# Performance work log

Hardware: AMD Instinct MI355X
Metric: run time of the kernel (lower is better)

Reference implementation:

```python
import jax, jax.numpy as jnp
import numpy as np

B, T, C = 16, 2048, 512
G = 2                 # groups
V = 320               # num_vars
D = C // G            # var_dim = 256
GAMMA = 0.25
GN_EPS = 1e-5


def setup_inputs() -> dict:
    key = jax.random.key(0)
    k1, k2, k3 = jax.random.split(key, 3)
    x = jax.random.normal(k1, (B, T, C), dtype=jnp.float32)
    # grouped 1x1 conv weight: (out_channels, in_channels_per_group) = (C, D)
    conv_w = jax.random.normal(k2, (C, D), dtype=jnp.float32) * (1.0 / np.sqrt(D))
    gn_w = jnp.ones((C,), dtype=jnp.float32)
    gn_b = jnp.zeros((C,), dtype=jnp.float32)
    embedding = 0.01 * jax.random.normal(k3, (V, G, D), dtype=jnp.float32)
    return {"x": x, "conv_w": conv_w, "gn_w": gn_w, "gn_b": gn_b, "embedding": embedding}


def reference(x, conv_w, gn_w, gn_b, embedding):
    # x: [B, T, C] (time_first=True) -> [B, C, T]
    xt = jnp.transpose(x, (0, 2, 1))
    # grouped 1x1 conv == per-group matmul
    xg = xt.reshape(B, G, D, T)                      # [B, G, D_in, T]
    wg = conv_w.reshape(G, D, D)                     # [G, D_out, D_in]
    h = jnp.einsum('bgit,goi->bgot', xg, wg)         # [B, G, D, T]
    # Fp32GroupNorm over (D, T) per (B, G)
    mu = h.mean(axis=(2, 3), keepdims=True)
    var = ((h - mu) ** 2).mean(axis=(2, 3), keepdims=True)
    hn = (h - mu) * jax.lax.rsqrt(var + GN_EPS)
    ze = hn.reshape(B, C, T) * gn_w[None, :, None] + gn_b[None, :, None]  # [B, C, T]

    ze_ = ze.reshape(B, G, D, T).transpose(0, 3, 1, 2)  # [B, T, G, D]
    # squared distances to codebook (same argmin as L2 norm)
    e_sq = (embedding ** 2).sum(-1).T                    # [G, V]
    d2 = ((ze_ ** 2).sum(-1)[..., None]
          - 2.0 * jnp.einsum('btgd,vgd->btgv', ze_, embedding)
          + e_sq[None, None])                            # [B, T, G, V]
    idx = jnp.argmin(d2, axis=-1)                        # [B, T, G] int32

    zq = embedding[idx, jnp.arange(G)[None, None, :]]    # [B, T, G, D]
    zq = zq.reshape(B, T, C).transpose(0, 2, 1)          # [B, C, T]

    # straight-through
    x_st = jax.lax.stop_gradient(zq) + (ze - jax.lax.stop_gradient(ze))
    x_out = jnp.transpose(x_st, (0, 2, 1))               # back to [B, T, C]

    # code perplexity from one-hot usage counts
    flat_idx = idx.reshape(-1, G)                        # [B*T, G]
    counts = jnp.zeros((V, G), dtype=jnp.float32).at[flat_idx, jnp.arange(G)[None, :]].add(1.0)
    hard_probs = counts.T / jnp.float32(B * T)           # [G, V]
    code_perplexity = jnp.exp(-jnp.sum(hard_probs * jnp.log(hard_probs + 1e-7), axis=-1)).sum()

    latent_loss = jnp.mean((zq - jax.lax.stop_gradient(ze)) ** 2)
    commitment_loss = jnp.mean((ze - jax.lax.stop_gradient(zq)) ** 2)
    kmeans_loss = latent_loss + GAMMA * commitment_loss
    return x_out, kmeans_loss, code_perplexity
```

## Files before the change

kernel.cpp:

```cpp
#include <hip/hip_runtime.h>
#include <math.h>

#define BB 16
#define TT 2048
#define CC 512
#define GG 2
#define DD 256
#define VV 320
#define DT (DD*TT)
#define NOUT ((size_t)BB*TT*CC)

#define OFF_H      0ULL
#define SZ_H       ((size_t)BB*GG*TT*DD*4)
#define OFF_PART   (OFF_H + SZ_H)
#define OFF_MUSIG  (OFF_PART + 4096ULL*2*8)
#define OFF_ESQ    (OFF_MUSIG + 32ULL*2*4)
#define OFF_CNT    (OFF_ESQ + (size_t)GG*VV*4)
#define OFF_LOSS   (OFF_CNT + (size_t)GG*VV*4)
#define OFF_EMBH   67180032ULL
#define OFF_WH     (OFF_EMBH + 327680ULL)
#define OFF_WL     (OFF_WH + 262144ULL)

typedef _Float16 half8   __attribute__((ext_vector_type(8)));
typedef float    f32x4   __attribute__((ext_vector_type(4)));

#define MARGIN 2e-3f
#define CAP 16

#define GLOAD_LDS16(g, l) \
  __builtin_amdgcn_global_load_lds((const __attribute__((address_space(1))) void*)(g), \
                                   (__attribute__((address_space(3))) void*)(l), 16, 0, 0)

__global__ __launch_bounds__(256) void k_emb(const float* __restrict__ emb,
                                             const float* __restrict__ w,
                                             _Float16* __restrict__ embHp,
                                             _Float16* __restrict__ wHp,
                                             _Float16* __restrict__ wLp,
                                             float* __restrict__ esq,
                                             unsigned* __restrict__ counts,
                                             float* __restrict__ loss) {
  int blk = blockIdx.x;
  int tid = threadIdx.x;
  if (blk == 40) {
    for (int i = tid; i < GG*VV; i += 256) counts[i] = 0u;
    if (tid == 0) *loss = 0.0f;
    return;
  }
  if (blk >= 41) {
    int wblk = blk - 41;
    int g = wblk >> 3, c = wblk & 7;
    int o = tid;
    const float* wrow = w + (size_t)(g*DD + o)*DD + (c << 5);
    #pragma unroll
    for (int hgrp = 0; hgrp < 4; ++hgrp) {
      float4 f1 = *(const float4*)(wrow + (hgrp << 2));
      float4 f2 = *(const float4*)(wrow + (hgrp << 2) + 16);
      float fv[8] = {f1.x, f1.y, f1.z, f1.w, f2.x, f2.y, f2.z, f2.w};
      half8 vh, vl;
      #pragma unroll
      for (int e = 0; e < 8; ++e) {
        _Float16 hh = (_Float16)fv[e];
        vh[e] = hh;
        vl[e] = (_Float16)(fv[e] - (float)hh);
      }
      size_t base = (((((size_t)(g*8 + c)) << 2) + hgrp) << 8) + o;
      *(half8*)(wHp + (base << 3)) = vh;
      *(half8*)(wLp + (base << 3)) = vl;
    }
    return;
  }
  int g = blk / 20;
  int v0 = (blk % 20) * 16;
  int vl = tid >> 4, dl = tid & 15;
  int v = v0 + vl;
  double sq = 0.0;
  #pragma unroll
  for (int k = 0; k < 16; k++) {
    int d = dl + (k << 4);
    float e = emb[((size_t)v*GG + g)*DD + d];
    sq += (double)e * (double)e;
  }
  #pragma unroll
  for (int m = 1; m < 16; m <<= 1) sq += __shfl_xor(sq, m);
  if (dl == 0) esq[g*VV + v] = (float)sq;

  const int hgrp = dl >> 2, jb = dl & 3;
  #pragma unroll
  for (int c = 0; c < 8; ++c) {
    int k0 = (c << 5) + (hgrp << 2) + jb;
    int k1 = k0 + 16;
    float e0 = emb[((size_t)v*GG + g)*DD + k0];
    float e1 = emb[((size_t)v*GG + g)*DD + k1];
    size_t base = (((size_t)(g*8 + c)*4 + hgrp)*320 + v)*8;
    embHp[base + jb]     = (_Float16)e0;
    embHp[base + jb + 4] = (_Float16)e1;
  }
}

__global__ __launch_bounds__(256, 2) void k_conv2(const float* __restrict__ x,
                                                  const _Float16* __restrict__ wH,
                                                  const _Float16* __restrict__ wL,
                                                  float* __restrict__ h,
                                                  double* __restrict__ part) {
  __shared__ __align__(16) char BsC[65536];
  __shared__ double r1[4], r2[4];
  const int bid = blockIdx.x;
  const int bg = bid >> 4, tt = bid & 15;
  const int b = bg >> 1, g = bg & 1;
  const int tid = threadIdx.x;
  const int wv = tid >> 6, lane = tid & 63;
  const int l15 = tid & 15, lh = lane >> 4;
  const int t0w = (tt << 7) + (wv << 5);

  f32x4 acc[2][16];
  #pragma unroll
  for (int tf = 0; tf < 2; ++tf)
    #pragma unroll
    for (int vf = 0; vf < 16; ++vf) acc[tf][vf] = 0.0f;

  const char* WHg = (const char*)(wH + ((size_t)g << 16));
  const char* WLg = (const char*)(wL + ((size_t)g << 16));
  const float* xb0 = x + ((size_t)(b*TT + t0w + l15)*CC + g*DD + (lh << 2));
  const float* xb1 = xb0 + ((size_t)16)*CC;

  {
    const char* sH = WHg + wv*4096 + lane*16;
    const char* sL = WLg + wv*4096 + lane*16;
    char* dH = BsC + wv*4096;
    char* dL = BsC + 32768 + wv*4096;
    #pragma unroll
    for (int i = 0; i < 4; ++i) {
      GLOAD_LDS16(sH + i*1024, dH + i*1024);
      GLOAD_LDS16(sL + i*1024, dL + i*1024);
    }
  }
  float4 p00 = *(const float4*)(xb0);
  float4 p01 = *(const float4*)(xb0 + 16);
  float4 p10 = *(const float4*)(xb1);
  float4 p11 = *(const float4*)(xb1 + 16);

  int cur = 0;
  #pragma unroll 1
  for (int c = 0; c < 8; ++c) {
    if (c < 7) {
      const char* sH = WHg + (size_t)(c + 1)*16384 + wv*4096 + lane*16;
      const char* sL = WLg + (size_t)(c + 1)*16384 + wv*4096 + lane*16;
      char* dH = BsC + (cur ^ 1)*16384 + wv*4096;
      char* dL = BsC + 32768 + (cur ^ 1)*16384 + wv*4096;
      #pragma unroll
      for (int i = 0; i < 4; ++i) {
        GLOAD_LDS16(sH + i*1024, dH + i*1024);
        GLOAD_LDS16(sL + i*1024, dL + i*1024);
      }
      asm volatile("s_waitcnt vmcnt(12)" ::: "memory");
    } else {
      asm volatile("s_waitcnt vmcnt(4)" ::: "memory");
    }
    __builtin_amdgcn_s_barrier();

    float4 c00 = p00, c01 = p01, c10 = p10, c11 = p11;
    if (c < 7) {
      const int off = (c + 1) << 5;
      p00 = *(const float4*)(xb0 + off);
      p01 = *(const float4*)(xb0 + off + 16);
      p10 = *(const float4*)(xb1 + off);
      p11 = *(const float4*)(xb1 + off + 16);
    }
    half8 ah[2], al[2];
    {
      float fv0[8] = {c00.x, c00.y, c00.z, c00.w, c01.x, c01.y, c01.z, c01.w};
      float fv1[8] = {c10.x, c10.y, c10.z, c10.w, c11.x, c11.y, c11.z, c11.w};
      #pragma unroll
      for (int e = 0; e < 8; ++e) {
        _Float16 h0 = (_Float16)fv0[e];
        ah[0][e] = h0; al[0][e] = (_Float16)(fv0[e] - (float)h0);
        _Float16 h1 = (_Float16)fv1[e];
        ah[1][e] = h1; al[1][e] = (_Float16)(fv1[e] - (float)h1);
      }
    }
    const char* BH = BsC + cur*16384;
    const char* BL = BsC + 32768 + cur*16384;
    #pragma unroll
    for (int vf = 0; vf < 16; ++vf) {
      const int o = (vf << 4) + l15;
      const int bo = ((lh << 8) + o) << 4;
      half8 bh = *(const half8*)(BH + bo);
      half8 bl = *(const half8*)(BL + bo);
      #pragma unroll
      for (int tf = 0; tf < 2; ++tf) {
        acc[tf][vf] = __builtin_amdgcn_mfma_f32_16x16x32_f16(ah[tf], bh, acc[tf][vf], 0, 0, 0);
        acc[tf][vf] = __builtin_amdgcn_mfma_f32_16x16x32_f16(al[tf], bh, acc[tf][vf], 0, 0, 0);
        acc[tf][vf] = __builtin_amdgcn_mfma_f32_16x16x32_f16(ah[tf], bl, acc[tf][vf], 0, 0, 0);
      }
    }
    __builtin_amdgcn_s_barrier();
    cur ^= 1;
  }

  double s1 = 0.0, s2 = 0.0;
  {
    float* hb = h + (size_t)bg*TT*DD;
    #pragma unroll
    for (int tf = 0; tf < 2; ++tf) {
      #pragma unroll
      for (int reg = 0; reg < 4; ++reg) {
        const int t = t0w + (tf << 4) + (lh << 2) + reg;
        float* hrow = hb + (size_t)t*DD + l15;
        #pragma unroll
        for (int vf = 0; vf < 16; ++vf) {
          float v = acc[tf][vf][reg];
          hrow[vf << 4] = v;
          double dv = (double)v;
          s1 += dv; s2 += dv*dv;
        }
      }
    }
  }
  #pragma unroll
  for (int m = 32; m > 0; m >>= 1) { s1 += __shfl_down(s1, m); s2 += __shfl_down(s2, m); }
  if (lane == 0) { r1[wv] = s1; r2[wv] = s2; }
  __syncthreads();
  if (tid == 0) {
    part[(size_t)bid*2]     = r1[0] + r1[1] + r1[2] + r1[3];
    part[(size_t)bid*2 + 1] = r2[0] + r2[1] + r2[2] + r2[3];
  }
}

__global__ __launch_bounds__(256, 2) void k_vq2(const float* __restrict__ h,
                                                const double* __restrict__ part,
                                                const float* __restrict__ gn_w,
                                                const float* __restrict__ gn_b,
                                                const _Float16* __restrict__ embH,
                                                const float* __restrict__ esq,
                                                const float* __restrict__ emb,
                                                float* __restrict__ out,
                                                unsigned* __restrict__ counts,
                                                float* __restrict__ loss) {
  __shared__ __align__(16) char smem[43008];
  float*  esqs    = (float*)smem;
  int*    candcnt = (int*)(smem + 1280);
  int*    bestv   = (int*)(smem + 1792);
  int*    slowl   = (int*)(smem + 2304);
  int*    nslow   = (int*)(smem + 2816);
  float*  ze2s    = (float*)(smem + 2880);
  float*  ymins   = (float*)(smem + 3392);
  float*  lossrow = (float*)(smem + 3904);
  unsigned short* cand = (unsigned short*)(smem + 4416);
  float*  gnws    = (float*)(smem + 40960);
  float*  gnbs    = (float*)(smem + 41984);

  const int bid = blockIdx.x;
  const int bg  = bid >> 4;
  const int t0  = (bid & 15) << 7;
  const int b = bg >> 1, g = bg & 1;
  const int tid = threadIdx.x;
  const int lane = tid & 63, wv = tid >> 6;
  const int l15 = tid & 15, lh = lane >> 4;

  float mu, rs;
  {
    double s1 = 0.0, s2 = 0.0;
    const double* pp = part + (size_t)bg*32;
    for (int r = 0; r < 16; r++) { s1 += pp[r*2]; s2 += pp[r*2 + 1]; }
    double mud = s1 / (double)DT;
    double var = s2 / (double)DT - mud*mud;
    double rsd = 1.0 / sqrt(var + 1e-5);
    mu = (float)mud;
    rs = (float)rsd;
  }

  const float* hb = h + ((size_t)bg*TT + t0)*DD;
  const char* gBH = (const char*)(embH + (size_t)(g*8)*10240);
  const float* gwp = gn_w + g*DD;
  const float* gbp = gn_b + g*DD;

  gnws[tid] = gwp[tid];
  gnbs[tid] = gbp[tid];
  __syncthreads();

  f32x4 acc[2][20];
  #pragma unroll
  for (int tf = 0; tf < 2; ++tf)
    #pragma unroll
    for (int vf = 0; vf < 20; ++vf) acc[tf][vf] = 0.0f;

  const float* hr0 = hb + (size_t)((wv << 5) + l15)*DD + (lh << 2);
  const float* hr1 = hr0 + ((size_t)16)*DD;

  {
    const char* sB = gBH + wv*5120 + lane*16;
    char* dB = smem + wv*5120;
    #pragma unroll
    for (int i = 0; i < 5; ++i) GLOAD_LDS16(sB + i*1024, dB + i*1024);
  }
  asm volatile("" ::: "memory");
  float4 a00 = *(const float4*)(hr0);
  float4 a01 = *(const float4*)(hr0 + 16);
  float4 a10 = *(const float4*)(hr1);
  float4 a11 = *(const float4*)(hr1 + 16);

  float ze2a0 = 0.0f, ze2a1 = 0.0f;
  #pragma unroll
  for (int c = 0; c < 8; ++c) {
    const int cu = c & 1;
    if (c < 7) {
      const char* sB = gBH + (size_t)(c + 1)*20480 + wv*5120 + lane*16;
      char* dB = smem + (cu ^ 1)*20480 + wv*5120;
      #pragma unroll
      for (int i = 0; i < 5; ++i) GLOAD_LDS16(sB + i*1024, dB + i*1024);
    }
    asm volatile("" ::: "memory");
    float4 n00, n01, n10, n11;
    if (c < 7) {
      const int off = (c + 1) << 5;
      n00 = *(const float4*)(hr0 + off);
      n01 = *(const float4*)(hr0 + off + 16);
      n10 = *(const float4*)(hr1 + off);
      n11 = *(const float4*)(hr1 + off + 16);
    }
    if (c < 7) { asm volatile("s_waitcnt vmcnt(13)" ::: "memory"); }
    else       { asm volatile("s_waitcnt vmcnt(4)"  ::: "memory"); }
    __builtin_amdgcn_s_barrier();

    const int c32 = c << 5;
    half8 ah[2];
    {
      float4 w1 = *(const float4*)(gnws + c32 + (lh << 2));
      float4 w2 = *(const float4*)(gnws + c32 + (lh << 2) + 16);
      float4 b1 = *(const float4*)(gnbs + c32 + (lh << 2));
      float4 b2 = *(const float4*)(gnbs + c32 + (lh << 2) + 16);
      float wv_[8] = {w1.x, w1.y, w1.z, w1.w, w2.x, w2.y, w2.z, w2.w};
      float bv_[8] = {b1.x, b1.y, b1.z, b1.w, b2.x, b2.y, b2.z, b2.w};
      float f0[8] = {a00.x, a00.y, a00.z, a00.w, a01.x, a01.y, a01.z, a01.w};
      float f1[8] = {a10.x, a10.y, a10.z, a10.w, a11.x, a11.y, a11.z, a11.w};
      #pragma unroll
      for (int e = 0; e < 8; ++e) {
        float z0 = __fmul_rn(__fsub_rn(f0[e], mu), rs);
        z0 = __fadd_rn(__fmul_rn(z0, wv_[e]), bv_[e]);
        ah[0][e] = (_Float16)z0;
        ze2a0 = fmaf(z0, z0, ze2a0);
        float z1 = __fmul_rn(__fsub_rn(f1[e], mu), rs);
        z1 = __fadd_rn(__fmul_rn(z1, wv_[e]), bv_[e]);
        ah[1][e] = (_Float16)z1;
        ze2a1 = fmaf(z1, z1, ze2a1);
      }
    }
    const char* BH = smem + cu*20480;
    #pragma unroll
    for (int vf = 0; vf < 20; ++vf) {
      const int v = (vf << 4) + l15;
      half8 bh = *(const half8*)(BH + ((lh*320 + v) << 4));
      acc[0][vf] = __builtin_amdgcn_mfma_f32_16x16x32_f16(ah[0], bh, acc[0][vf], 0, 0, 0);
      acc[1][vf] = __builtin_amdgcn_mfma_f32_16x16x32_f16(ah[1], bh, acc[1][vf], 0, 0, 0);
    }
    __builtin_amdgcn_s_barrier();
    if (c < 7) { a00 = n00; a01 = n01; a10 = n10; a11 = n11; }
  }
  __syncthreads();

  if (tid < 160) { esqs[tid] = esq[g*VV + tid]; esqs[tid + 160] = esq[g*VV + tid + 160]; }
  if (tid < 128) { candcnt[tid] = 0; bestv[tid] = -1; }
  if (tid == 0) *nslow = 0;
  {
    float s = ze2a0;
    s += __shfl_down(s, 32);
    s += __shfl_down(s, 16);
    if (lane < 16) ze2s[(wv << 5) + l15] = s;
    float t = ze2a1;
    t += __shfl_down(t, 32);
    t += __shfl_down(t, 16);
    if (lane < 16) ze2s[(wv << 5) + 16 + l15] = t;
  }
  __syncthreads();

  #pragma unroll
  for (int tf = 0; tf < 2; ++tf) {
    #pragma unroll
    for (int reg = 0; reg < 4; ++reg) {
      int row = (wv << 5) + (tf << 4) + (lh << 2) + reg;
      float y[20]; float mn = 3.4e38f;
      #pragma unroll
      for (int vf = 0; vf < 20; ++vf) {
        y[vf] = fmaf(-2.0f, acc[tf][vf][reg], esqs[(vf << 4) + l15]);
        mn = fminf(mn, y[vf]);
      }
      #pragma unroll
      for (int m = 1; m < 16; m <<= 1) mn = fminf(mn, __shfl_xor(mn, m));
      if (l15 == 0) ymins[row] = mn;
      float thr = mn + MARGIN;
      #pragma unroll
      for (int vf = 0; vf < 20; ++vf) {
        if (y[vf] <= thr) {
          int pos = atomicAdd(&candcnt[row], 1);
          if (pos < CAP) cand[row*CAP + pos] = (unsigned short)((vf << 4) + l15);
        }
      }
    }
  }
  __syncthreads();
  if (tid < 128) {
    int cnt = candcnt[tid];
    if (cnt == 1) {
      bestv[tid] = cand[tid*CAP];
      lossrow[tid] = ze2s[tid] + ymins[tid];
    } else {
      int p = atomicAdd(nslow, 1); slowl[p] = tid;
    }
  }
  __syncthreads();

  const int ns = *nslow;
  for (int i = wv; i < ns; i += 4) {
    const int row = slowl[i];
    float4 hx  = *(const float4*)(hb + (size_t)row*DD + (lane << 2));
    float4 gw4 = *(const float4*)(gwp + (lane << 2));
    float4 gb4 = *(const float4*)(gbp + (lane << 2));
    float hv[4] = {hx.x, hx.y, hx.z, hx.w};
    float gwv[4] = {gw4.x, gw4.y, gw4.z, gw4.w};
    float gbv[4] = {gb4.x, gb4.y, gb4.z, gb4.w};
    float zf[4];
    #pragma unroll
    for (int e = 0; e < 4; ++e) {
      float z = __fmul_rn(__fsub_rn(hv[e], mu), rs);
      zf[e] = __fadd_rn(__fmul_rn(z, gwv[e]), gbv[e]);
    }
    int cnt = candcnt[row];
    double bd = 1e300; int bvv = 0x7fffffff;
    if (cnt <= CAP) {
      for (int ci = 0; ci < cnt; ++ci) {
        int v = cand[row*CAP + ci];
        float4 ev = *(const float4*)(emb + ((size_t)v*GG + g)*DD + (lane << 2));
        float evv[4] = {ev.x, ev.y, ev.z, ev.w};
        double s = 0.0;
        #pragma unroll
        for (int e = 0; e < 4; ++e) {
          double df = (double)zf[e] - (double)evv[e];
          s += df*df;
        }
        #pragma unroll
        for (int m = 32; m > 0; m >>= 1) s += __shfl_down(s, m);
        s = __shfl(s, 0);
        if (s < bd || (s == bd && v < bvv)) { bd = s; bvv = v; }
      }
    } else {
      for (int v = 0; v < VV; ++v) {
        float4 ev = *(const float4*)(emb + ((size_t)v*GG + g)*DD + (lane << 2));
        float evv[4] = {ev.x, ev.y, ev.z, ev.w};
        double s = 0.0;
        #pragma unroll
        for (int e = 0; e < 4; ++e) {
          double df = (double)zf[e] - (double)evv[e];
          s += df*df;
        }
        #pragma unroll
        for (int m = 32; m > 0; m >>= 1) s += __shfl_down(s, m);
        s = __shfl(s, 0);
        if (s < bd) { bd = s; bvv = v; }
      }
    }
    if (lane == 0) { bestv[row] = bvv; lossrow[row] = (float)bd; }
  }
  __syncthreads();

  if (tid < 128) atomicAdd(&counts[g*VV + bestv[tid]], 1u);
  if (wv == 0) {
    float s = lossrow[lane] + lossrow[lane + 64];
    #pragma unroll
    for (int m = 32; m > 0; m >>= 1) s += __shfl_down(s, m);
    if (lane == 0) atomicAdd(loss, s);
  }

  float* ob = out + (size_t)(b*TT + t0)*CC + g*DD + tid;
  #pragma unroll 1
  for (int r0 = 0; r0 < 128; r0 += 8) {
    int vv[8]; float ee[8];
    #pragma unroll
    for (int j = 0; j < 8; ++j) vv[j] = bestv[r0 + j];
    #pragma unroll
    for (int j = 0; j < 8; ++j) ee[j] = emb[((size_t)vv[j]*GG + g)*DD + tid];
    #pragma unroll
    for (int j = 0; j < 8; ++j) ob[(size_t)(r0 + j)*CC] = ee[j];
  }
}

__global__ __launch_bounds__(256) void k_final(const unsigned* __restrict__ counts,
                                               const float* __restrict__ loss,
                                               float* __restrict__ out) {
  __shared__ float sd[256];
  int tid = threadIdx.x;
  float perp = 0.0f;
  for (int g = 0; g < GG; g++) {
    float p1 = 0.0f;
    for (int v = tid; v < VV; v += 256) {
      float p = (float)counts[g*VV + v] / 32768.0f;
      p1 += p * logf(p + 1e-7f);
    }
    sd[tid] = p1;
    __syncthreads();
    for (int s = 128; s > 0; s >>= 1) {
      if (tid < s) sd[tid] += sd[tid + s];
      __syncthreads();
    }
    if (tid == 0) perp += expf(-sd[0]);
    __syncthreads();
  }
  if (tid == 0) {
    out[NOUT]     = 1.25f * (*loss) / (float)NOUT;
    out[NOUT + 1] = perp;
  }
}

extern "C" void kernel_launch(void* const* d_in, const int* in_sizes, int n_in,
                              void* d_out, int out_size, void* d_ws, size_t ws_size,
                              hipStream_t stream) {
  const float* x   = (const float*)d_in[0];
  const float* cw  = (const float*)d_in[1];
  const float* gnw = (const float*)d_in[2];
  const float* gnb = (const float*)d_in[3];
  const float* emb = (const float*)d_in[4];
  float* out = (float*)d_out;
  char* ws = (char*)d_ws;
  float*     h      = (float*)(ws + OFF_H);
  double*    part   = (double*)(ws + OFF_PART);
  float*     esq    = (float*)(ws + OFF_ESQ);
  unsigned*  counts = (unsigned*)(ws + OFF_CNT);
  float*     loss   = (float*)(ws + OFF_LOSS);
  _Float16*  embH   = (_Float16*)(ws + OFF_EMBH);
  _Float16*  wH     = (_Float16*)(ws + OFF_WH);
  _Float16*  wL     = (_Float16*)(ws + OFF_WL);

  hipLaunchKernelGGL(k_emb,   dim3(57),   dim3(256), 0, stream,
                     emb, cw, embH, wH, wL, esq, counts, loss);
  hipLaunchKernelGGL(k_conv2, dim3(512),  dim3(256), 0, stream, x, wH, wL, h, part);
  hipLaunchKernelGGL(k_vq2,   dim3(512),  dim3(256), 0, stream,
                     h, part, gnw, gnb, embH, esq, emb, out, counts, loss);
  hipLaunchKernelGGL(k_final, dim3(1),    dim3(256), 0, stream, counts, loss, out);
}
```

Before: 98.13 us.

## Split VQ scoring from output gather into a separate write kernel

Moves the codebook-row gather and output write out of the scoring kernel into a new kernel that writes both groups of each row, using indices staged through a global buffer. The old per-block write covered only 1KB of each 2KB output row, strided by row. The new kernel writes full contiguous rows and runs with many more blocks, so the output store pattern should improve. The cost is an extra kernel launch plus a global index round-trip.

```diff
diff --git a/kernel.cpp b/kernel.cpp
--- a/kernel.cpp
+++ b/kernel.cpp
@@ -20,6 +20,7 @@
 #define OFF_EMBH   67180032ULL
 #define OFF_WH     (OFF_EMBH + 327680ULL)
 #define OFF_WL     (OFF_WH + 262144ULL)
+#define OFF_BESTV  (OFF_WL + 262144ULL)
 
 typedef _Float16 half8   __attribute__((ext_vector_type(8)));
 typedef float    f32x4   __attribute__((ext_vector_type(4)));
@@ -226,16 +227,16 @@
   }
 }
 
-__global__ __launch_bounds__(256, 2) void k_vq2(const float* __restrict__ h,
-                                                const double* __restrict__ part,
-                                                const float* __restrict__ gn_w,
-                                                const float* __restrict__ gn_b,
-                                                const _Float16* __restrict__ embH,
-                                                const float* __restrict__ esq,
-                                                const float* __restrict__ emb,
-                                                float* __restrict__ out,
-                                                unsigned* __restrict__ counts,
-                                                float* __restrict__ loss) {
+__global__ __launch_bounds__(256, 2) void k_score(const float* __restrict__ h,
+                                                  const double* __restrict__ part,
+                                                  const float* __restrict__ gn_w,
+                                                  const float* __restrict__ gn_b,
+                                                  const _Float16* __restrict__ embH,
+                                                  const float* __restrict__ esq,
+                                                  const float* __restrict__ emb,
+                                                  int* __restrict__ bestvW,
+                                                  unsigned* __restrict__ counts,
+                                                  float* __restrict__ loss) {
   __shared__ __align__(16) char smem[43008];
   float*  esqs    = (float*)smem;
   int*    candcnt = (int*)(smem + 1280);
@@ -252,7 +253,7 @@
   const int bid = blockIdx.x;
   const int bg  = bid >> 4;
   const int t0  = (bid & 15) << 7;
-  const int b = bg >> 1, g = bg & 1;
+  const int g = bg & 1;
   const int tid = threadIdx.x;
   const int lane = tid & 63, wv = tid >> 6;
   const int l15 = tid & 15, lh = lane >> 4;
@@ -470,16 +471,33 @@
     if (lane == 0) atomicAdd(loss, s);
   }
 
-  float* ob = out + (size_t)(b*TT + t0)*CC + g*DD + tid;
+  if (tid < 128) bestvW[(size_t)bg*TT + t0 + tid] = bestv[tid];
+}
+
+__global__ __launch_bounds__(256) void k_write(const int* __restrict__ bestvW,
+                                               const float* __restrict__ emb,
+                                               float* __restrict__ out) {
+  const int bid = blockIdx.x;
+  const int b = bid >> 7;
+  const int t0 = (bid & 127) << 4;
+  const int tid = threadIdx.x;
+  const int* bv0 = bestvW + (size_t)(b*2 + 0)*TT + t0;
+  const int* bv1 = bestvW + (size_t)(b*2 + 1)*TT + t0;
+  float* ob = out + ((size_t)(b*TT + t0))*CC;
   #pragma unroll 1
-  for (int r0 = 0; r0 < 128; r0 += 8) {
-    int vv[8]; float ee[8];
-    #pragma unroll
-    for (int j = 0; j < 8; ++j) vv[j] = bestv[r0 + j];
-    #pragma unroll
-    for (int j = 0; j < 8; ++j) ee[j] = emb[((size_t)vv[j]*GG + g)*DD + tid];
-    #pragma unroll
-    for (int j = 0; j < 8; ++j) ob[(size_t)(r0 + j)*CC] = ee[j];
+  for (int r0 = 0; r0 < 16; r0 += 4) {
+    int v0[4], v1[4]; float e0[4], e1[4];
+    #pragma unroll
+    for (int j = 0; j < 4; ++j) { v0[j] = bv0[r0 + j]; v1[j] = bv1[r0 + j]; }
+    #pragma unroll
+    for (int j = 0; j < 4; ++j) e0[j] = emb[((size_t)v0[j]*GG + 0)*DD + tid];
+    #pragma unroll
+    for (int j = 0; j < 4; ++j) e1[j] = emb[((size_t)v1[j]*GG + 1)*DD + tid];
+    #pragma unroll
+    for (int j = 0; j < 4; ++j) {
+      ob[(size_t)(r0 + j)*CC + tid]       = e0[j];
+      ob[(size_t)(r0 + j)*CC + 256 + tid] = e1[j];
+    }
   }
 }
 
@@ -528,11 +546,13 @@
   _Float16*  embH   = (_Float16*)(ws + OFF_EMBH);
   _Float16*  wH     = (_Float16*)(ws + OFF_WH);
   _Float16*  wL     = (_Float16*)(ws + OFF_WL);
+  int*       bestvW = (int*)(ws + OFF_BESTV);
 
   hipLaunchKernelGGL(k_emb,   dim3(57),   dim3(256), 0, stream,
                      emb, cw, embH, wH, wL, esq, counts, loss);
   hipLaunchKernelGGL(k_conv2, dim3(512),  dim3(256), 0, stream, x, wH, wL, h, part);
-  hipLaunchKernelGGL(k_vq2,   dim3(512),  dim3(256), 0, stream,
-                     h, part, gnw, gnb, embH, esq, emb, out, counts, loss);
+  hipLaunchKernelGGL(k_score, dim3(512),  dim3(256), 0, stream,
+                     h, part, gnw, gnb, embH, esq, emb, bestvW, counts, loss);
+  hipLaunchKernelGGL(k_write, dim3(2048), dim3(256), 0, stream, bestvW, emb, out);
   hipLaunchKernelGGL(k_final, dim3(1),    dim3(256), 0, stream, counts, loss, out);
 }
```

After: 101.8 us. +3.8%, slower.
